# Kernel tuning notes

Measured on AMD Instinct MI355X. Metric: run time of the kernel, lower is better.

The kernel has to match this reference:

```python
import jax, jax.numpy as jnp
import numpy as np

B, L, D, H = 1024, 77, 1024, 16
DFF = 4096


def setup_inputs() -> dict:
    key = jax.random.key(0)
    ks = jax.random.split(key, 26)
    w = lambda k, shape: jax.random.normal(k, shape, jnp.float32) * 0.02
    z = lambda n: jnp.zeros((n,), jnp.float32)
    return {
        "x": jax.random.normal(ks[0], (B, D), jnp.float32),
        "t_emb": jax.random.normal(ks[1], (B, D), jnp.float32),
        "context_seq": jax.random.normal(ks[2], (B, L, D), jnp.float32),
        "context_padding_mask": jnp.zeros((B, L), dtype=bool),
        "w_mod": w(ks[3], (9 * D, D)), "b_mod": z(9 * D),
        "sa_wq": w(ks[4], (D, D)), "sa_bq": z(D),
        "sa_wk": w(ks[5], (D, D)), "sa_bk": z(D),
        "sa_wv": w(ks[6], (D, D)), "sa_bv": z(D),
        "sa_wo": w(ks[7], (D, D)), "sa_bo": z(D),
        "ca_wq": w(ks[8], (D, D)), "ca_bq": z(D),
        "ca_wk": w(ks[9], (D, D)), "ca_bk": z(D),
        "ca_wv": w(ks[10], (D, D)), "ca_bv": z(D),
        "ca_wo": w(ks[11], (D, D)), "ca_bo": z(D),
        "w1": w(ks[12], (DFF, D)), "b1": z(DFF),
        "w2": w(ks[13], (DFF, DFF)), "b2": z(DFF),
        "w3": w(ks[14], (D, DFF)), "b3": z(D),
        "num_heads": H,
    }


def _ln(x, eps=1e-6):
    # LayerNorm without affine params (elementwise_affine=False)
    m = jnp.mean(x, axis=-1, keepdims=True)
    v = jnp.mean(jnp.square(x - m), axis=-1, keepdims=True)
    return (x - m) / jnp.sqrt(v + eps)


def _mha(qx, kx, vx, wq, bq, wk, bk, wv, bv, wo, bo, h, key_padding_mask=None):
    # qx: [B, Lq, D], kx/vx: [B, Lk, D]; torch MultiheadAttention math
    Bb, Lq, Dm = qx.shape
    Lk = kx.shape[1]
    dh = Dm // h
    q = (qx @ wq.T + bq).reshape(Bb, Lq, h, dh).transpose(0, 2, 1, 3)
    k = (kx @ wk.T + bk).reshape(Bb, Lk, h, dh).transpose(0, 2, 1, 3)
    v = (vx @ wv.T + bv).reshape(Bb, Lk, h, dh).transpose(0, 2, 1, 3)
    scores = jnp.einsum("bhqd,bhkd->bhqk", q, k) / jnp.sqrt(jnp.asarray(dh, qx.dtype))
    if key_padding_mask is not None:
        # True means "ignore this key"
        scores = jnp.where(key_padding_mask[:, None, None, :], jnp.asarray(-1e9, qx.dtype), scores)
    attn = jax.nn.softmax(scores, axis=-1)
    out = jnp.einsum("bhqk,bhkd->bhqd", attn, v)
    out = out.transpose(0, 2, 1, 3).reshape(Bb, Lq, Dm)
    return out @ wo.T + bo


def reference(x, t_emb, context_seq, context_padding_mask,
              w_mod, b_mod,
              sa_wq, sa_bq, sa_wk, sa_bk, sa_wv, sa_bv, sa_wo, sa_bo,
              ca_wq, ca_bq, ca_wk, ca_bk, ca_wv, ca_bv, ca_wo, ca_bo,
              w1, b1, w2, b2, w3, b3, num_heads):
    # AdaLN-zero modulation parameters
    mod = jax.nn.silu(t_emb) @ w_mod.T + b_mod  # [B, 9D]
    g1, be1, a1, g2, be2, a2, g3, be3, a3 = jnp.split(mod, 9, axis=1)

    x_q = x[:, None, :]  # [B, 1, D]

    # self-attention branch (seq_len = 1)
    m1 = _ln(x_q) * (1.0 + g1[:, None, :]) + be1[:, None, :]
    sa = _mha(m1, m1, m1, sa_wq, sa_bq, sa_wk, sa_bk, sa_wv, sa_bv, sa_wo, sa_bo, num_heads)
    x_q = x_q + a1[:, None, :] * sa

    # cross-attention branch
    m2 = _ln(x_q) * (1.0 + g2[:, None, :]) + be2[:, None, :]
    ca = _mha(m2, context_seq, context_seq, ca_wq, ca_bq, ca_wk, ca_bk, ca_wv, ca_bv,
              ca_wo, ca_bo, num_heads, key_padding_mask=context_padding_mask)
    x_q = x_q + a2[:, None, :] * ca

    # MLP branch (3-layer, exact GELU as nn.GELU default)
    m3 = _ln(x_q) * (1.0 + g3[:, None, :]) + be3[:, None, :]
    hdn = jax.nn.gelu(m3 @ w1.T + b1, approximate=False)
    hdn = jax.nn.gelu(hdn @ w2.T + b2, approximate=False)
    ff = hdn @ w3.T + b3
    x_q = x_q + a3[:, None, :] * ff

    return x_q[:, 0, :]
```

## Files before the change

### kernel.cpp

```cpp
#include <hip/hip_runtime.h>
#include <cmath>
#include <stdint.h>


#define DD 1024
#define NB 1024
#define LK 77
#define NHEAD 16
#define DFF_ 4096

typedef __bf16 bf16_t;
typedef __attribute__((ext_vector_type(8))) __bf16 bf16x8;
typedef __attribute__((ext_vector_type(4))) __bf16 bf16x4v;
typedef __attribute__((ext_vector_type(4))) float f32x4;

__global__ __launch_bounds__(256) void k_f2b(const float* __restrict__ in,
                                             bf16_t* __restrict__ out, int n) {
    int i = (blockIdx.x * 256 + threadIdx.x) * 4;
    if (i + 3 < n) {
        float4 v = *(const float4*)(in + i);
        bf16x4v o;
        o[0] = (bf16_t)v.x; o[1] = (bf16_t)v.y; o[2] = (bf16_t)v.z; o[3] = (bf16_t)v.w;
        *(bf16x4v*)(out + i) = o;
    }
}

__global__ __launch_bounds__(256) void k_silu_f2b(const float* __restrict__ in,
                                                  bf16_t* __restrict__ out, int n) {
    int i = (blockIdx.x * 256 + threadIdx.x) * 4;
    if (i + 3 < n) {
        float4 v = *(const float4*)(in + i);
        bf16x4v o;
        o[0] = (bf16_t)(v.x / (1.0f + __expf(-v.x)));
        o[1] = (bf16_t)(v.y / (1.0f + __expf(-v.y)));
        o[2] = (bf16_t)(v.z / (1.0f + __expf(-v.z)));
        o[3] = (bf16_t)(v.w / (1.0f + __expf(-v.w)));
        *(bf16x4v*)(out + i) = o;
    }
}

__global__ __launch_bounds__(256) void k_transpose_f2b(const float* __restrict__ in,
                                                       bf16_t* __restrict__ out) {
    __shared__ float t[32][33];
    int lx = threadIdx.x & 31, ly = threadIdx.x >> 5;
    int bx = blockIdx.x * 32, by = blockIdx.y * 32;
#pragma unroll
    for (int r = 0; r < 4; ++r)
        t[ly + r * 8][lx] = in[(size_t)(by + ly + r * 8) * DD + bx + lx];
    __syncthreads();
#pragma unroll
    for (int r = 0; r < 4; ++r)
        out[(size_t)(bx + ly + r * 8) * DD + by + lx] = (bf16_t)t[lx][ly + r * 8];
}

__global__ __launch_bounds__(256) void k_ln_mod(const float* __restrict__ x,
                                                const float* __restrict__ mod,
                                                int gOff, int beOff,
                                                bf16_t* __restrict__ out) {
    const int b = blockIdx.x;
    const int t = threadIdx.x;
    const float4 v = *(const float4*)(x + (size_t)b * DD + t * 4);
    float s = v.x + v.y + v.z + v.w;
    float q = v.x * v.x + v.y * v.y + v.z * v.z + v.w * v.w;
#pragma unroll
    for (int o = 32; o > 0; o >>= 1) {
        s += __shfl_xor(s, o, 64);
        q += __shfl_xor(q, o, 64);
    }
    __shared__ float rs[4], rq[4];
    const int w = t >> 6;
    if ((t & 63) == 0) { rs[w] = s; rq[w] = q; }
    __syncthreads();
    const float S = rs[0] + rs[1] + rs[2] + rs[3];
    const float Q = rq[0] + rq[1] + rq[2] + rq[3];
    const float mean = S * (1.0f / DD);
    const float var = Q * (1.0f / DD) - mean * mean;
    const float rstd = rsqrtf(var + 1e-6f);
    const float* mrow = mod + (size_t)b * (9 * DD);
    const float4 g = *(const float4*)(mrow + gOff + t * 4);
    const float4 e = *(const float4*)(mrow + beOff + t * 4);
    bf16x4v o;
    o[0] = (bf16_t)((v.x - mean) * rstd * (1.0f + g.x) + e.x);
    o[1] = (bf16_t)((v.y - mean) * rstd * (1.0f + g.y) + e.y);
    o[2] = (bf16_t)((v.z - mean) * rstd * (1.0f + g.z) + e.z);
    o[3] = (bf16_t)((v.w - mean) * rstd * (1.0f + g.w) + e.w);
    *(bf16x4v*)(out + (size_t)b * DD + t * 4) = o;
}

template <int BN, bool GELU_E, bool RESID, bool WF32, bool WB16>
__global__ __launch_bounds__(256) void k_gemm(
    const bf16_t* __restrict__ A, int lda, int aHeadOff,
    const bf16_t* __restrict__ W, int ldw, int wHeadOff,
    const float* __restrict__ bias, int biasHeadOff,
    float* __restrict__ Cf, bf16_t* __restrict__ Cb, int ldc, int cHeadOff,
    const float* __restrict__ res, int ldres,
    const float* __restrict__ am, int ldam,
    int K) {
    constexpr int BM = 128, BK = 32;
    const int z = blockIdx.z;
    A += (size_t)z * aHeadOff;
    W += (size_t)z * wHeadOff;
    const float* biasz = bias ? bias + (size_t)z * biasHeadOff : nullptr;
    const size_t coff = (size_t)z * cHeadOff;

    __shared__ bf16_t As[BM * BK];
    __shared__ bf16_t Bs[BN * BK];

    const int tid = threadIdx.x;
    const int wave = tid >> 6, lane = tid & 63;
    const int m0 = blockIdx.y * BM, n0 = blockIdx.x * BN;
    const int wm = (wave >> 1) * 64;
    constexpr int WN = (BN == 128) ? 64 : 32;
    const int wn = (wave & 1) * WN;
    constexpr int FN = WN / 16;

    f32x4 acc[4][FN];
#pragma unroll
    for (int i = 0; i < 4; ++i)
#pragma unroll
        for (int j = 0; j < FN; ++j) acc[i][j] = {0.f, 0.f, 0.f, 0.f};

    const int lrow = lane & 15;
    const int lk8 = (lane >> 4) * 8;

    for (int k0 = 0; k0 < K; k0 += BK) {
        const int c0 = tid, c1 = tid + 256;
        bf16x8 ta0 = *(const bf16x8*)(A + (size_t)(m0 + (c0 >> 2)) * lda + k0 + (c0 & 3) * 8);
        bf16x8 ta1 = *(const bf16x8*)(A + (size_t)(m0 + (c1 >> 2)) * lda + k0 + (c1 & 3) * 8);
        bf16x8 tb0 = *(const bf16x8*)(W + (size_t)(n0 + (c0 >> 2)) * ldw + k0 + (c0 & 3) * 8);
        bf16x8 tb1;
        if constexpr (BN == 128)
            tb1 = *(const bf16x8*)(W + (size_t)(n0 + (c1 >> 2)) * ldw + k0 + (c1 & 3) * 8);

        __syncthreads();
        *(bf16x8*)(As + c0 * 8) = ta0;
        *(bf16x8*)(As + c1 * 8) = ta1;
        *(bf16x8*)(Bs + c0 * 8) = tb0;
        if constexpr (BN == 128) *(bf16x8*)(Bs + c1 * 8) = tb1;
        __syncthreads();

        bf16x8 af[4], bfr[FN];
#pragma unroll
        for (int i = 0; i < 4; ++i)
            af[i] = *(const bf16x8*)(As + (wm + i * 16 + lrow) * BK + lk8);
#pragma unroll
        for (int j = 0; j < FN; ++j)
            bfr[j] = *(const bf16x8*)(Bs + (wn + j * 16 + lrow) * BK + lk8);
#pragma unroll
        for (int i = 0; i < 4; ++i)
#pragma unroll
            for (int j = 0; j < FN; ++j)
                acc[i][j] = __builtin_amdgcn_mfma_f32_16x16x32_bf16(af[i], bfr[j], acc[i][j], 0, 0, 0);
    }

    const int r4 = (lane >> 4) * 4;
    const int cc = lane & 15;
#pragma unroll
    for (int i = 0; i < 4; ++i) {
#pragma unroll
        for (int j = 0; j < FN; ++j) {
            const int col = n0 + wn + j * 16 + cc;
            const float bv = biasz ? biasz[col] : 0.0f;
#pragma unroll
            for (int e = 0; e < 4; ++e) {
                const int row = m0 + wm + i * 16 + r4 + e;
                float v = acc[i][j][e] + bv;
                if constexpr (GELU_E) v = 0.5f * v * (1.0f + erff(v * 0.70710678118654752f));
                const size_t cidx = coff + (size_t)row * ldc + col;
                if constexpr (RESID) {
                    Cf[cidx] = res[(size_t)row * ldres + col] + am[(size_t)row * ldam + col] * v;
                } else {
                    if constexpr (WF32) Cf[cidx] = v;
                    if constexpr (WB16) Cb[cidx] = (bf16_t)v;
                }
            }
        }
    }
}

__global__ __launch_bounds__(64) void k_qbk(const bf16_t* __restrict__ q,
                                            const float* __restrict__ bk,
                                            float* __restrict__ qbk) {
    const int b = blockIdx.x, lane = threadIdx.x;
#pragma unroll 1
    for (int h = 0; h < NHEAD; ++h) {
        float v = (float)q[(size_t)b * DD + h * 64 + lane] * bk[h * 64 + lane];
#pragma unroll
        for (int o = 32; o > 0; o >>= 1) v += __shfl_xor(v, o, 64);
        if (lane == 0) qbk[(size_t)b * NHEAD + h] = v;
    }
}

__global__ __launch_bounds__(256) void k_ca_scores(
    const bf16_t* __restrict__ qt, const float* __restrict__ qbk,
    const float* __restrict__ ctx, const unsigned char* __restrict__ mask,
    float* __restrict__ p) {
    constexpr int QS = DD + 8;
    constexpr int CS = DD + 8;
    __shared__ unsigned short qlds[NHEAD * QS];
    __shared__ float clds[4 * CS];
    __shared__ float slds[NHEAD * 80];
    __shared__ float plds[4 * NHEAD * 4];

    const int b = blockIdx.x;
    const int t = threadIdx.x;
    const unsigned short* qg = (const unsigned short*)(qt + (size_t)b * (NHEAD * DD));
    for (int e = t; e < NHEAD * DD; e += 256) {
        int h = e >> 10, d = e & (DD - 1);
        qlds[h * QS + d] = qg[e];
    }

    const int h = t & 15;
    const int lc = (t >> 4) & 3;
    const int dq = t >> 6;

    for (int c0 = 0; c0 < LK; c0 += 4) {
        __syncthreads();
        {
            int i = t >> 6;
            int dcol = (t & 63) * 16;
            int l = c0 + i;
            if (l < LK) {
                const float* src = ctx + ((size_t)b * LK + l) * DD + dcol;
                float* dst = clds + i * CS + dcol;
#pragma unroll
                for (int u = 0; u < 4; ++u) *(f32x4*)(dst + u * 4) = *(const f32x4*)(src + u * 4);
            }
        }
        __syncthreads();
        int l = c0 + lc;
        float part = 0.0f;
        if (l < LK) {
            const unsigned short* qr = qlds + h * QS + dq * 256;
            const float* cr = clds + lc * CS + dq * 256;
#pragma unroll 4
            for (int d = 0; d < 256; d += 8) {
                bf16x8 qv = *(const bf16x8*)(qr + d);
                f32x4 ca = *(const f32x4*)(cr + d);
                f32x4 cb = *(const f32x4*)(cr + d + 4);
                part += (float)qv[0] * ca.x + (float)qv[1] * ca.y + (float)qv[2] * ca.z +
                        (float)qv[3] * ca.w + (float)qv[4] * cb.x + (float)qv[5] * cb.y +
                        (float)qv[6] * cb.z + (float)qv[7] * cb.w;
            }
        }
        plds[(dq * NHEAD + h) * 4 + lc] = part;
        __syncthreads();
        if (t < 64) {
            int hh = t & 15, ll = t >> 4;
            int lg = c0 + ll;
            if (lg < LK) {
                float s = plds[(0 * NHEAD + hh) * 4 + ll] + plds[(1 * NHEAD + hh) * 4 + ll] +
                          plds[(2 * NHEAD + hh) * 4 + ll] + plds[(3 * NHEAD + hh) * 4 + ll];
                s = (s + qbk[(size_t)b * NHEAD + hh]) * 0.125f;
                if (mask[(size_t)b * LK + lg]) s = -1.0e9f;
                slds[hh * 80 + lg] = s;
            }
        }
    }
    __syncthreads();
    if (t < NHEAD) {
        float mx = -3.0e38f;
#pragma unroll 1
        for (int l2 = 0; l2 < LK; ++l2) mx = fmaxf(mx, slds[t * 80 + l2]);
        float sum = 0.0f;
#pragma unroll 1
        for (int l2 = 0; l2 < LK; ++l2) {
            float e2 = __expf(slds[t * 80 + l2] - mx);
            slds[t * 80 + l2] = e2;
            sum += e2;
        }
        float inv = 1.0f / sum;
#pragma unroll 1
        for (int l2 = 0; l2 < LK; ++l2)
            p[((size_t)b * NHEAD + t) * LK + l2] = slds[t * 80 + l2] * inv;
    }
}

__global__ __launch_bounds__(256) void k_ca_mix(const float* __restrict__ p,
                                                const float* __restrict__ ctx,
                                                bf16_t* __restrict__ mixed) {
    __shared__ float plds[NHEAD * LK];
    __shared__ float clds[4 * DD];
    const int b = blockIdx.x;
    const int t = threadIdx.x;
    for (int e = t; e < NHEAD * LK; e += 256) plds[e] = p[(size_t)b * NHEAD * LK + e];
    const int h = t >> 4, dseg = t & 15;
    f32x4 acc4[16];
#pragma unroll
    for (int j = 0; j < 16; ++j) acc4[j] = {0.f, 0.f, 0.f, 0.f};
    for (int c0 = 0; c0 < LK; c0 += 4) {
        __syncthreads();
        {
            int i = t >> 6;
            int dcol = (t & 63) * 16;
            int l = c0 + i;
            if (l < LK) {
                const float* src = ctx + ((size_t)b * LK + l) * DD + dcol;
                float* dst = clds + i * DD + dcol;
#pragma unroll
                for (int u = 0; u < 4; ++u) *(f32x4*)(dst + u * 4) = *(const f32x4*)(src + u * 4);
            }
        }
        __syncthreads();
#pragma unroll
        for (int lc2 = 0; lc2 < 4; ++lc2) {
            int l = c0 + lc2;
            if (l < LK) {
                float pl = plds[h * LK + l];
                const float* cr = clds + lc2 * DD + dseg * 4;
#pragma unroll
                for (int j = 0; j < 16; ++j) {
                    f32x4 cv = *(const f32x4*)(cr + j * 64);
                    acc4[j].x += pl * cv.x;
                    acc4[j].y += pl * cv.y;
                    acc4[j].z += pl * cv.z;
                    acc4[j].w += pl * cv.w;
                }
            }
        }
    }
    bf16_t* orow = mixed + ((size_t)b * NHEAD + h) * DD + dseg * 4;
#pragma unroll
    for (int j = 0; j < 16; ++j) {
        bf16x4v o;
        o[0] = (bf16_t)acc4[j].x; o[1] = (bf16_t)acc4[j].y;
        o[2] = (bf16_t)acc4[j].z; o[3] = (bf16_t)acc4[j].w;
        *(bf16x4v*)(orow + j * 64) = o;
    }
}

extern "C" void kernel_launch(void* const* d_in, const int* in_sizes, int n_in,
                              void* d_out, int out_size, void* d_ws, size_t ws_size,
                              hipStream_t stream) {
    const float* x = (const float*)d_in[0];
    const float* temb = (const float*)d_in[1];
    const float* ctx = (const float*)d_in[2];
    const unsigned char* mask = (const unsigned char*)d_in[3];
    const float* w_mod = (const float*)d_in[4];
    const float* b_mod = (const float*)d_in[5];
    const float* sa_wv = (const float*)d_in[10];
    const float* sa_bv = (const float*)d_in[11];
    const float* sa_wo = (const float*)d_in[12];
    const float* sa_bo = (const float*)d_in[13];
    const float* ca_wq = (const float*)d_in[14];
    const float* ca_bq = (const float*)d_in[15];
    const float* ca_wk = (const float*)d_in[16];
    const float* ca_bk = (const float*)d_in[17];
    const float* ca_wv = (const float*)d_in[18];
    const float* ca_bv = (const float*)d_in[19];
    const float* ca_wo = (const float*)d_in[20];
    const float* ca_bo = (const float*)d_in[21];
    const float* w1 = (const float*)d_in[22];
    const float* b1 = (const float*)d_in[23];
    const float* w2 = (const float*)d_in[24];
    const float* b2 = (const float*)d_in[25];
    const float* w3 = (const float*)d_in[26];
    const float* b3 = (const float*)d_in[27];

    char* ws = (char*)d_ws;
    size_t off = 0;
    auto alloc = [&](size_t bytes) -> void* {
        void* pp = ws + off;
        off += (bytes + 255) & ~(size_t)255;
        return pp;
    };
    bf16_t* w_mod_b = (bf16_t*)alloc((size_t)9 * DD * DD * 2);
    bf16_t* sa_wv_b = (bf16_t*)alloc((size_t)DD * DD * 2);
    bf16_t* sa_wo_b = (bf16_t*)alloc((size_t)DD * DD * 2);
    bf16_t* ca_wq_b = (bf16_t*)alloc((size_t)DD * DD * 2);
    bf16_t* ca_wv_b = (bf16_t*)alloc((size_t)DD * DD * 2);
    bf16_t* ca_wo_b = (bf16_t*)alloc((size_t)DD * DD * 2);
    bf16_t* wkT_b = (bf16_t*)alloc((size_t)DD * DD * 2);
    bf16_t* w1_b = (bf16_t*)alloc((size_t)DFF_ * DD * 2);
    bf16_t* w2_b = (bf16_t*)alloc((size_t)DFF_ * DFF_ * 2);
    bf16_t* w3_b = (bf16_t*)alloc((size_t)DD * DFF_ * 2);
    bf16_t* tb = (bf16_t*)alloc((size_t)NB * DD * 2);
    float* mod_f = (float*)alloc((size_t)NB * 9 * DD * 4);
    bf16_t* m_b = (bf16_t*)alloc((size_t)NB * DD * 2);
    bf16_t* vsa_b = (bf16_t*)alloc((size_t)NB * DD * 2);
    float* x1 = (float*)alloc((size_t)NB * DD * 4);
    float* x2 = (float*)alloc((size_t)NB * DD * 4);
    bf16_t* q_b = (bf16_t*)alloc((size_t)NB * DD * 2);
    bf16_t* qt_b = (bf16_t*)alloc((size_t)NB * NHEAD * DD * 2);
    float* qbk_f = (float*)alloc((size_t)NB * NHEAD * 4);
    float* p_f = (float*)alloc((size_t)NB * NHEAD * LK * 4);
    bf16_t* oh_b = (bf16_t*)alloc((size_t)NB * DD * 2);
    bf16_t* h1_b = (bf16_t*)alloc((size_t)NB * DFF_ * 2);
    bf16_t* h2_b = (bf16_t*)alloc((size_t)NB * DFF_ * 2);
    bf16_t* mixed_b = qt_b;
    (void)n_in; (void)in_sizes; (void)out_size; (void)ws_size;

    dim3 blk(256);
    k_f2b<<<9 * DD * DD / 1024, blk, 0, stream>>>(w_mod, w_mod_b, 9 * DD * DD);
    k_f2b<<<DD * DD / 1024, blk, 0, stream>>>(sa_wv, sa_wv_b, DD * DD);
    k_f2b<<<DD * DD / 1024, blk, 0, stream>>>(sa_wo, sa_wo_b, DD * DD);
    k_f2b<<<DD * DD / 1024, blk, 0, stream>>>(ca_wq, ca_wq_b, DD * DD);
    k_f2b<<<DD * DD / 1024, blk, 0, stream>>>(ca_wv, ca_wv_b, DD * DD);
    k_f2b<<<DD * DD / 1024, blk, 0, stream>>>(ca_wo, ca_wo_b, DD * DD);
    k_f2b<<<DFF_ * DD / 1024, blk, 0, stream>>>(w1, w1_b, DFF_ * DD);
    k_f2b<<<DFF_ * DFF_ / 1024, blk, 0, stream>>>(w2, w2_b, DFF_ * DFF_);
    k_f2b<<<DFF_ * DD / 1024, blk, 0, stream>>>(w3, w3_b, DFF_ * DD);
    k_transpose_f2b<<<dim3(32, 32), blk, 0, stream>>>(ca_wk, wkT_b);
    k_silu_f2b<<<NB * DD / 1024, blk, 0, stream>>>(temb, tb, NB * DD);

    k_gemm<128, false, false, true, false><<<dim3(9 * DD / 128, NB / 128, 1), blk, 0, stream>>>(
        tb, DD, 0, w_mod_b, DD, 0, b_mod, 0, mod_f, nullptr, 9 * DD, 0, nullptr, 0, nullptr, 0, DD);

    k_ln_mod<<<NB, blk, 0, stream>>>(x, mod_f, 0 * DD, 1 * DD, m_b);
    k_gemm<128, false, false, false, true><<<dim3(8, 8, 1), blk, 0, stream>>>(
        m_b, DD, 0, sa_wv_b, DD, 0, sa_bv, 0, nullptr, vsa_b, DD, 0, nullptr, 0, nullptr, 0, DD);
    k_gemm<128, false, true, true, false><<<dim3(8, 8, 1), blk, 0, stream>>>(
        vsa_b, DD, 0, sa_wo_b, DD, 0, sa_bo, 0, x1, nullptr, DD, 0, x, DD, mod_f + 2 * DD, 9 * DD, DD);

    k_ln_mod<<<NB, blk, 0, stream>>>(x1, mod_f, 3 * DD, 4 * DD, m_b);
    k_gemm<128, false, false, false, true><<<dim3(8, 8, 1), blk, 0, stream>>>(
        m_b, DD, 0, ca_wq_b, DD, 0, ca_bq, 0, nullptr, q_b, DD, 0, nullptr, 0, nullptr, 0, DD);
    k_gemm<128, false, false, false, true><<<dim3(8, 8, 16), blk, 0, stream>>>(
        q_b, DD, 64, wkT_b, DD, 64, nullptr, 0, nullptr, qt_b, NHEAD * DD, DD, nullptr, 0, nullptr, 0, 64);
    k_qbk<<<NB, 64, 0, stream>>>(q_b, ca_bk, qbk_f);
    k_ca_scores<<<NB, blk, 0, stream>>>(qt_b, qbk_f, ctx, mask, p_f);
    k_ca_mix<<<NB, blk, 0, stream>>>(p_f, ctx, mixed_b);
    k_gemm<64, false, false, false, true><<<dim3(1, 8, 16), blk, 0, stream>>>(
        mixed_b, NHEAD * DD, DD, ca_wv_b, DD, 64 * DD, ca_bv, 64, nullptr, oh_b, DD, 64,
        nullptr, 0, nullptr, 0, DD);
    k_gemm<128, false, true, true, false><<<dim3(8, 8, 1), blk, 0, stream>>>(
        oh_b, DD, 0, ca_wo_b, DD, 0, ca_bo, 0, x2, nullptr, DD, 0, x1, DD, mod_f + 5 * DD, 9 * DD, DD);

    k_ln_mod<<<NB, blk, 0, stream>>>(x2, mod_f, 6 * DD, 7 * DD, m_b);
    k_gemm<128, true, false, false, true><<<dim3(DFF_ / 128, 8, 1), blk, 0, stream>>>(
        m_b, DD, 0, w1_b, DD, 0, b1, 0, nullptr, h1_b, DFF_, 0, nullptr, 0, nullptr, 0, DD);
    k_gemm<128, true, false, false, true><<<dim3(DFF_ / 128, 8, 1), blk, 0, stream>>>(
        h1_b, DFF_, 0, w2_b, DFF_, 0, b2, 0, nullptr, h2_b, DFF_, 0, nullptr, 0, nullptr, 0, DFF_);
    k_gemm<128, false, true, true, false><<<dim3(8, 8, 1), blk, 0, stream>>>(
        h2_b, DFF_, 0, w3_b, DFF_, 0, b3, 0, (float*)d_out, nullptr, DD, 0, x2, DD,
        mod_f + 8 * DD, 9 * DD, DFF_);
}
```

Measured before the change: 1.251 ms.

## Fuse cross-attention into online-softmax kernel, batch weight casts, retile GEMMs with direct LDS loads

```diff
diff --git a/kernel.cpp b/kernel.cpp
--- a/kernel.cpp
+++ b/kernel.cpp
@@ -14,29 +14,31 @@
 typedef __attribute__((ext_vector_type(4))) __bf16 bf16x4v;
 typedef __attribute__((ext_vector_type(4))) float f32x4;
 
-__global__ __launch_bounds__(256) void k_f2b(const float* __restrict__ in,
-                                             bf16_t* __restrict__ out, int n) {
-    int i = (blockIdx.x * 256 + threadIdx.x) * 4;
-    if (i + 3 < n) {
-        float4 v = *(const float4*)(in + i);
-        bf16x4v o;
-        o[0] = (bf16_t)v.x; o[1] = (bf16_t)v.y; o[2] = (bf16_t)v.z; o[3] = (bf16_t)v.w;
-        *(bf16x4v*)(out + i) = o;
-    }
-}
-
-__global__ __launch_bounds__(256) void k_silu_f2b(const float* __restrict__ in,
-                                                  bf16_t* __restrict__ out, int n) {
-    int i = (blockIdx.x * 256 + threadIdx.x) * 4;
-    if (i + 3 < n) {
-        float4 v = *(const float4*)(in + i);
-        bf16x4v o;
-        o[0] = (bf16_t)(v.x / (1.0f + __expf(-v.x)));
-        o[1] = (bf16_t)(v.y / (1.0f + __expf(-v.y)));
-        o[2] = (bf16_t)(v.z / (1.0f + __expf(-v.z)));
-        o[3] = (bf16_t)(v.w / (1.0f + __expf(-v.w)));
-        *(bf16x4v*)(out + i) = o;
-    }
+__device__ __forceinline__ void gload16(const bf16_t* g, bf16_t* l) {
+    __builtin_amdgcn_global_load_lds(
+        (const __attribute__((address_space(1))) void*)g,
+        (__attribute__((address_space(3))) void*)l, 16, 0, 0);
+}
+
+struct ConvTab {
+    const float* src[40];
+    bf16_t* dst[40];
+    int silu[40];
+};
+
+__global__ __launch_bounds__(256) void k_conv_all(ConvTab tab) {
+    const int u = blockIdx.x >> 10;
+    const int i = ((blockIdx.x & 1023) * 256 + threadIdx.x) * 4;
+    float4 v = *(const float4*)(tab.src[u] + i);
+    if (tab.silu[u]) {
+        v.x = v.x / (1.0f + __expf(-v.x));
+        v.y = v.y / (1.0f + __expf(-v.y));
+        v.z = v.z / (1.0f + __expf(-v.z));
+        v.w = v.w / (1.0f + __expf(-v.w));
+    }
+    bf16x4v o;
+    o[0] = (bf16_t)v.x; o[1] = (bf16_t)v.y; o[2] = (bf16_t)v.z; o[3] = (bf16_t)v.w;
+    *(bf16x4v*)(tab.dst[u] + i) = o;
 }
 
 __global__ __launch_bounds__(256) void k_transpose_f2b(const float* __restrict__ in,
@@ -87,7 +89,7 @@
     *(bf16x4v*)(out + (size_t)b * DD + t * 4) = o;
 }
 
-template <int BN, bool GELU_E, bool RESID, bool WF32, bool WB16>
+template <int BM, int BN, bool GELU_E, bool RESID, bool WF32, bool WB16>
 __global__ __launch_bounds__(256) void k_gemm(
     const bf16_t* __restrict__ A, int lda, int aHeadOff,
     const bf16_t* __restrict__ W, int ldw, int wHeadOff,
@@ -96,7 +98,10 @@
     const float* __restrict__ res, int ldres,
     const float* __restrict__ am, int ldam,
     int K) {
-    constexpr int BM = 128, BK = 32;
+    constexpr int BK = 32;
+    constexpr int FM = BM / 32, FN = BN / 32;
+    constexpr int CA_ = (BM * BK) / 2048;
+    constexpr int CB_ = (BN * BK) / 2048;
     const int z = blockIdx.z;
     A += (size_t)z * aHeadOff;
     W += (size_t)z * wHeadOff;
@@ -109,14 +114,12 @@
     const int tid = threadIdx.x;
     const int wave = tid >> 6, lane = tid & 63;
     const int m0 = blockIdx.y * BM, n0 = blockIdx.x * BN;
-    const int wm = (wave >> 1) * 64;
-    constexpr int WN = (BN == 128) ? 64 : 32;
-    const int wn = (wave & 1) * WN;
-    constexpr int FN = WN / 16;
-
-    f32x4 acc[4][FN];
-#pragma unroll
-    for (int i = 0; i < 4; ++i)
+    const int wm = (wave >> 1) * (BM / 2);
+    const int wn = (wave & 1) * (BN / 2);
+
+    f32x4 acc[FM][FN];
+#pragma unroll
+    for (int i = 0; i < FM; ++i)
 #pragma unroll
         for (int j = 0; j < FN; ++j) acc[i][j] = {0.f, 0.f, 0.f, 0.f};
 
@@ -124,30 +127,28 @@
     const int lk8 = (lane >> 4) * 8;
 
     for (int k0 = 0; k0 < K; k0 += BK) {
-        const int c0 = tid, c1 = tid + 256;
-        bf16x8 ta0 = *(const bf16x8*)(A + (size_t)(m0 + (c0 >> 2)) * lda + k0 + (c0 & 3) * 8);
-        bf16x8 ta1 = *(const bf16x8*)(A + (size_t)(m0 + (c1 >> 2)) * lda + k0 + (c1 & 3) * 8);
-        bf16x8 tb0 = *(const bf16x8*)(W + (size_t)(n0 + (c0 >> 2)) * ldw + k0 + (c0 & 3) * 8);
-        bf16x8 tb1;
-        if constexpr (BN == 128)
-            tb1 = *(const bf16x8*)(W + (size_t)(n0 + (c1 >> 2)) * ldw + k0 + (c1 & 3) * 8);
-
-        __syncthreads();
-        *(bf16x8*)(As + c0 * 8) = ta0;
-        *(bf16x8*)(As + c1 * 8) = ta1;
-        *(bf16x8*)(Bs + c0 * 8) = tb0;
-        if constexpr (BN == 128) *(bf16x8*)(Bs + c1 * 8) = tb1;
-        __syncthreads();
-
-        bf16x8 af[4], bfr[FN];
-#pragma unroll
-        for (int i = 0; i < 4; ++i)
+        __syncthreads();
+#pragma unroll
+        for (int c = 0; c < CA_; ++c) {
+            const int e = (c * 256 + tid) * 8;
+            gload16(A + (size_t)(m0 + (e >> 5)) * lda + k0 + (e & 31), As + e);
+        }
+#pragma unroll
+        for (int c = 0; c < CB_; ++c) {
+            const int e = (c * 256 + tid) * 8;
+            gload16(W + (size_t)(n0 + (e >> 5)) * ldw + k0 + (e & 31), Bs + e);
+        }
+        __syncthreads();
+
+        bf16x8 af[FM], bfr[FN];
+#pragma unroll
+        for (int i = 0; i < FM; ++i)
             af[i] = *(const bf16x8*)(As + (wm + i * 16 + lrow) * BK + lk8);
 #pragma unroll
         for (int j = 0; j < FN; ++j)
             bfr[j] = *(const bf16x8*)(Bs + (wn + j * 16 + lrow) * BK + lk8);
 #pragma unroll
-        for (int i = 0; i < 4; ++i)
+        for (int i = 0; i < FM; ++i)
 #pragma unroll
             for (int j = 0; j < FN; ++j)
                 acc[i][j] = __builtin_amdgcn_mfma_f32_16x16x32_bf16(af[i], bfr[j], acc[i][j], 0, 0, 0);
@@ -156,7 +157,7 @@
     const int r4 = (lane >> 4) * 4;
     const int cc = lane & 15;
 #pragma unroll
-    for (int i = 0; i < 4; ++i) {
+    for (int i = 0; i < FM; ++i) {
 #pragma unroll
         for (int j = 0; j < FN; ++j) {
             const int col = n0 + wn + j * 16 + cc;
@@ -191,141 +192,133 @@
     }
 }
 
-__global__ __launch_bounds__(256) void k_ca_scores(
+#define CQS 1032
+__global__ __launch_bounds__(256) void k_ca_fused(
     const bf16_t* __restrict__ qt, const float* __restrict__ qbk,
     const float* __restrict__ ctx, const unsigned char* __restrict__ mask,
-    float* __restrict__ p) {
-    constexpr int QS = DD + 8;
-    constexpr int CS = DD + 8;
-    __shared__ unsigned short qlds[NHEAD * QS];
-    __shared__ float clds[4 * CS];
-    __shared__ float slds[NHEAD * 80];
-    __shared__ float plds[4 * NHEAD * 4];
+    bf16_t* __restrict__ mixed) {
+    __shared__ bf16_t qs[16 * CQS];
+    __shared__ bf16_t cs[8 * CQS];
+    __shared__ float plds[2 * 16 * 8];
+    __shared__ float wex[16 * 8];
+    __shared__ float fs[16];
+    __shared__ float inv[16];
 
     const int b = blockIdx.x;
     const int t = threadIdx.x;
-    const unsigned short* qg = (const unsigned short*)(qt + (size_t)b * (NHEAD * DD));
-    for (int e = t; e < NHEAD * DD; e += 256) {
-        int h = e >> 10, d = e & (DD - 1);
-        qlds[h * QS + d] = qg[e];
-    }
-
-    const int h = t & 15;
-    const int lc = (t >> 4) & 3;
-    const int dq = t >> 6;
-
-    for (int c0 = 0; c0 < LK; c0 += 4) {
+
+    {
+        const int h = t >> 4, dl = (t & 15) * 8;
+        const bf16_t* src = qt + ((size_t)b * 16 + h) * DD;
+#pragma unroll
+        for (int u = 0; u < 8; ++u)
+            *(bf16x8*)(qs + h * CQS + dl + u * 128) = *(const bf16x8*)(src + dl + u * 128);
+    }
+
+    const int hD = t & 15, l3D = (t >> 4) & 7, dq = t >> 7;
+    const int hM = t >> 4, ds16 = t & 15;
+    float acc[8][8];
+#pragma unroll
+    for (int j = 0; j < 8; ++j)
+#pragma unroll
+        for (int e = 0; e < 8; ++e) acc[j][e] = 0.f;
+
+    float mrun = -3.0e38f, den = 0.f;
+    const float qb = (t < 16) ? qbk[(size_t)b * NHEAD + t] : 0.f;
+
+    for (int c0 = 0; c0 < LK; c0 += 8) {
         __syncthreads();
         {
-            int i = t >> 6;
-            int dcol = (t & 63) * 16;
-            int l = c0 + i;
-            if (l < LK) {
-                const float* src = ctx + ((size_t)b * LK + l) * DD + dcol;
-                float* dst = clds + i * CS + dcol;
-#pragma unroll
-                for (int u = 0; u < 4; ++u) *(f32x4*)(dst + u * 4) = *(const f32x4*)(src + u * 4);
-            }
-        }
-        __syncthreads();
-        int l = c0 + lc;
-        float part = 0.0f;
-        if (l < LK) {
-            const unsigned short* qr = qlds + h * QS + dq * 256;
-            const float* cr = clds + lc * CS + dq * 256;
-#pragma unroll 4
-            for (int d = 0; d < 256; d += 8) {
-                bf16x8 qv = *(const bf16x8*)(qr + d);
-                f32x4 ca = *(const f32x4*)(cr + d);
-                f32x4 cb = *(const f32x4*)(cr + d + 4);
-                part += (float)qv[0] * ca.x + (float)qv[1] * ca.y + (float)qv[2] * ca.z +
-                        (float)qv[3] * ca.w + (float)qv[4] * cb.x + (float)qv[5] * cb.y +
-                        (float)qv[6] * cb.z + (float)qv[7] * cb.w;
-            }
-        }
-        plds[(dq * NHEAD + h) * 4 + lc] = part;
-        __syncthreads();
-        if (t < 64) {
-            int hh = t & 15, ll = t >> 4;
-            int lg = c0 + ll;
+            const int l = t >> 5, d4 = (t & 31) * 4;
+            const int lg = c0 + l;
             if (lg < LK) {
-                float s = plds[(0 * NHEAD + hh) * 4 + ll] + plds[(1 * NHEAD + hh) * 4 + ll] +
-                          plds[(2 * NHEAD + hh) * 4 + ll] + plds[(3 * NHEAD + hh) * 4 + ll];
-                s = (s + qbk[(size_t)b * NHEAD + hh]) * 0.125f;
-                if (mask[(size_t)b * LK + lg]) s = -1.0e9f;
-                slds[hh * 80 + lg] = s;
+                const float* src = ctx + ((size_t)b * LK + lg) * DD;
+#pragma unroll
+                for (int u = 0; u < 8; ++u) {
+                    f32x4 v = *(const f32x4*)(src + d4 + u * 128);
+                    bf16x4v o;
+                    o[0] = (bf16_t)v.x; o[1] = (bf16_t)v.y;
+                    o[2] = (bf16_t)v.z; o[3] = (bf16_t)v.w;
+                    *(bf16x4v*)(cs + l * CQS + d4 + u * 128) = o;
+                }
+            } else {
+                bf16x4v o = {(bf16_t)0.f, (bf16_t)0.f, (bf16_t)0.f, (bf16_t)0.f};
+#pragma unroll
+                for (int u = 0; u < 8; ++u) *(bf16x4v*)(cs + l * CQS + d4 + u * 128) = o;
+            }
+        }
+        __syncthreads();
+        {
+            float part = 0.f;
+            const bf16_t* qr = qs + hD * CQS + dq * 512;
+            const bf16_t* cr = cs + l3D * CQS + dq * 512;
+#pragma unroll 8
+            for (int i = 0; i < 64; ++i) {
+                bf16x8 qv = *(const bf16x8*)(qr + i * 8);
+                bf16x8 cv = *(const bf16x8*)(cr + i * 8);
+#pragma unroll
+                for (int e = 0; e < 8; ++e) part += (float)qv[e] * (float)cv[e];
+            }
+            plds[dq * 128 + hD * 8 + l3D] = part;
+        }
+        __syncthreads();
+        if (t < 16) {
+            float s[8];
+            float cm = -3.0e38f;
+#pragma unroll
+            for (int l = 0; l < 8; ++l) {
+                const int lg = c0 + l;
+                float sv = -3.0e38f;
+                if (lg < LK) {
+                    sv = (plds[t * 8 + l] + plds[128 + t * 8 + l] + qb) * 0.125f;
+                    if (mask[(size_t)b * LK + lg]) sv = -1.0e9f;
+                }
+                s[l] = sv;
+                cm = fmaxf(cm, sv);
+            }
+            const float mnew = fmaxf(mrun, cm);
+            const float f = __expf(mrun - mnew);
+            float wsum = 0.f;
+#pragma unroll
+            for (int l = 0; l < 8; ++l) {
+                const float w = (c0 + l < LK) ? __expf(s[l] - mnew) : 0.f;
+                wex[t * 8 + l] = w;
+                wsum += w;
+            }
+            den = den * f + wsum;
+            mrun = mnew;
+            fs[t] = f;
+            inv[t] = 1.0f / den;
+        }
+        __syncthreads();
+        {
+            const float f = fs[hM];
+#pragma unroll
+            for (int j = 0; j < 8; ++j)
+#pragma unroll
+                for (int e = 0; e < 8; ++e) acc[j][e] *= f;
+#pragma unroll
+            for (int l = 0; l < 8; ++l) {
+                const float w = wex[hM * 8 + l];
+                const bf16_t* cr = cs + l * CQS + ds16 * 8;
+#pragma unroll
+                for (int j = 0; j < 8; ++j) {
+                    bf16x8 cv = *(const bf16x8*)(cr + j * 128);
+#pragma unroll
+                    for (int e = 0; e < 8; ++e) acc[j][e] += w * (float)cv[e];
+                }
             }
         }
     }
     __syncthreads();
-    if (t < NHEAD) {
-        float mx = -3.0e38f;
-#pragma unroll 1
-        for (int l2 = 0; l2 < LK; ++l2) mx = fmaxf(mx, slds[t * 80 + l2]);
-        float sum = 0.0f;
-#pragma unroll 1
-        for (int l2 = 0; l2 < LK; ++l2) {
-            float e2 = __expf(slds[t * 80 + l2] - mx);
-            slds[t * 80 + l2] = e2;
-            sum += e2;
-        }
-        float inv = 1.0f / sum;
-#pragma unroll 1
-        for (int l2 = 0; l2 < LK; ++l2)
-            p[((size_t)b * NHEAD + t) * LK + l2] = slds[t * 80 + l2] * inv;
-    }
-}
-
-__global__ __launch_bounds__(256) void k_ca_mix(const float* __restrict__ p,
-                                                const float* __restrict__ ctx,
-                                                bf16_t* __restrict__ mixed) {
-    __shared__ float plds[NHEAD * LK];
-    __shared__ float clds[4 * DD];
-    const int b = blockIdx.x;
-    const int t = threadIdx.x;
-    for (int e = t; e < NHEAD * LK; e += 256) plds[e] = p[(size_t)b * NHEAD * LK + e];
-    const int h = t >> 4, dseg = t & 15;
-    f32x4 acc4[16];
-#pragma unroll
-    for (int j = 0; j < 16; ++j) acc4[j] = {0.f, 0.f, 0.f, 0.f};
-    for (int c0 = 0; c0 < LK; c0 += 4) {
-        __syncthreads();
-        {
-            int i = t >> 6;
-            int dcol = (t & 63) * 16;
-            int l = c0 + i;
-            if (l < LK) {
-                const float* src = ctx + ((size_t)b * LK + l) * DD + dcol;
-                float* dst = clds + i * DD + dcol;
-#pragma unroll
-                for (int u = 0; u < 4; ++u) *(f32x4*)(dst + u * 4) = *(const f32x4*)(src + u * 4);
-            }
-        }
-        __syncthreads();
-#pragma unroll
-        for (int lc2 = 0; lc2 < 4; ++lc2) {
-            int l = c0 + lc2;
-            if (l < LK) {
-                float pl = plds[h * LK + l];
-                const float* cr = clds + lc2 * DD + dseg * 4;
-#pragma unroll
-                for (int j = 0; j < 16; ++j) {
-                    f32x4 cv = *(const f32x4*)(cr + j * 64);
-                    acc4[j].x += pl * cv.x;
-                    acc4[j].y += pl * cv.y;
-                    acc4[j].z += pl * cv.z;
-                    acc4[j].w += pl * cv.w;
-                }
-            }
-        }
-    }
-    bf16_t* orow = mixed + ((size_t)b * NHEAD + h) * DD + dseg * 4;
-#pragma unroll
-    for (int j = 0; j < 16; ++j) {
-        bf16x4v o;
-        o[0] = (bf16_t)acc4[j].x; o[1] = (bf16_t)acc4[j].y;
-        o[2] = (bf16_t)acc4[j].z; o[3] = (bf16_t)acc4[j].w;
-        *(bf16x4v*)(orow + j * 64) = o;
+    const float iv = inv[hM];
+    bf16_t* orow = mixed + ((size_t)b * NHEAD + hM) * DD + ds16 * 8;
+#pragma unroll
+    for (int j = 0; j < 8; ++j) {
+        bf16x8 o;
+#pragma unroll
+        for (int e = 0; e < 8; ++e) o[e] = (bf16_t)(acc[j][e] * iv);
+        *(bf16x8*)(orow + j * 128) = o;
     }
 }
 
@@ -383,7 +376,6 @@
     bf16_t* q_b = (bf16_t*)alloc((size_t)NB * DD * 2);
     bf16_t* qt_b = (bf16_t*)alloc((size_t)NB * NHEAD * DD * 2);
     float* qbk_f = (float*)alloc((size_t)NB * NHEAD * 4);
-    float* p_f = (float*)alloc((size_t)NB * NHEAD * LK * 4);
     bf16_t* oh_b = (bf16_t*)alloc((size_t)NB * DD * 2);
     bf16_t* h1_b = (bf16_t*)alloc((size_t)NB * DFF_ * 2);
     bf16_t* h2_b = (bf16_t*)alloc((size_t)NB * DFF_ * 2);
@@ -391,47 +383,57 @@
     (void)n_in; (void)in_sizes; (void)out_size; (void)ws_size;
 
     dim3 blk(256);
-    k_f2b<<<9 * DD * DD / 1024, blk, 0, stream>>>(w_mod, w_mod_b, 9 * DD * DD);
-    k_f2b<<<DD * DD / 1024, blk, 0, stream>>>(sa_wv, sa_wv_b, DD * DD);
-    k_f2b<<<DD * DD / 1024, blk, 0, stream>>>(sa_wo, sa_wo_b, DD * DD);
-    k_f2b<<<DD * DD / 1024, blk, 0, stream>>>(ca_wq, ca_wq_b, DD * DD);
-    k_f2b<<<DD * DD / 1024, blk, 0, stream>>>(ca_wv, ca_wv_b, DD * DD);
-    k_f2b<<<DD * DD / 1024, blk, 0, stream>>>(ca_wo, ca_wo_b, DD * DD);
-    k_f2b<<<DFF_ * DD / 1024, blk, 0, stream>>>(w1, w1_b, DFF_ * DD);
-    k_f2b<<<DFF_ * DFF_ / 1024, blk, 0, stream>>>(w2, w2_b, DFF_ * DFF_);
-    k_f2b<<<DFF_ * DD / 1024, blk, 0, stream>>>(w3, w3_b, DFF_ * DD);
+    ConvTab tab{};
+    int nu = 0;
+    auto addseg = [&](const float* s, bf16_t* d, int units, int silu) {
+        for (int k = 0; k < units; ++k) {
+            tab.src[nu] = s + (size_t)k * 1048576;
+            tab.dst[nu] = d + (size_t)k * 1048576;
+            tab.silu[nu] = silu;
+            ++nu;
+        }
+    };
+    addseg(w_mod, w_mod_b, 9, 0);
+    addseg(sa_wv, sa_wv_b, 1, 0);
+    addseg(sa_wo, sa_wo_b, 1, 0);
+    addseg(ca_wq, ca_wq_b, 1, 0);
+    addseg(ca_wv, ca_wv_b, 1, 0);
+    addseg(ca_wo, ca_wo_b, 1, 0);
+    addseg(w1, w1_b, 4, 0);
+    addseg(w2, w2_b, 16, 0);
+    addseg(w3, w3_b, 4, 0);
+    addseg(temb, tb, 1, 1);
+    k_conv_all<<<nu * 1024, blk, 0, stream>>>(tab);
     k_transpose_f2b<<<dim3(32, 32), blk, 0, stream>>>(ca_wk, wkT_b);
-    k_silu_f2b<<<NB * DD / 1024, blk, 0, stream>>>(temb, tb, NB * DD);
-
-    k_gemm<128, false, false, true, false><<<dim3(9 * DD / 128, NB / 128, 1), blk, 0, stream>>>(
+
+    k_gemm<128, 128, false, false, true, false><<<dim3(72, 8, 1), blk, 0, stream>>>(
         tb, DD, 0, w_mod_b, DD, 0, b_mod, 0, mod_f, nullptr, 9 * DD, 0, nullptr, 0, nullptr, 0, DD);
 
     k_ln_mod<<<NB, blk, 0, stream>>>(x, mod_f, 0 * DD, 1 * DD, m_b);
-    k_gemm<128, false, false, false, true><<<dim3(8, 8, 1), blk, 0, stream>>>(
+    k_gemm<64, 64, false, false, false, true><<<dim3(16, 16, 1), blk, 0, stream>>>(
         m_b, DD, 0, sa_wv_b, DD, 0, sa_bv, 0, nullptr, vsa_b, DD, 0, nullptr, 0, nullptr, 0, DD);
-    k_gemm<128, false, true, true, false><<<dim3(8, 8, 1), blk, 0, stream>>>(
+    k_gemm<64, 64, false, true, true, false><<<dim3(16, 16, 1), blk, 0, stream>>>(
         vsa_b, DD, 0, sa_wo_b, DD, 0, sa_bo, 0, x1, nullptr, DD, 0, x, DD, mod_f + 2 * DD, 9 * DD, DD);
 
     k_ln_mod<<<NB, blk, 0, stream>>>(x1, mod_f, 3 * DD, 4 * DD, m_b);
-    k_gemm<128, false, false, false, true><<<dim3(8, 8, 1), blk, 0, stream>>>(
+    k_gemm<64, 64, false, false, false, true><<<dim3(16, 16, 1), blk, 0, stream>>>(
         m_b, DD, 0, ca_wq_b, DD, 0, ca_bq, 0, nullptr, q_b, DD, 0, nullptr, 0, nullptr, 0, DD);
-    k_gemm<128, false, false, false, true><<<dim3(8, 8, 16), blk, 0, stream>>>(
+    k_gemm<64, 64, false, false, false, true><<<dim3(16, 16, 16), blk, 0, stream>>>(
         q_b, DD, 64, wkT_b, DD, 64, nullptr, 0, nullptr, qt_b, NHEAD * DD, DD, nullptr, 0, nullptr, 0, 64);
     k_qbk<<<NB, 64, 0, stream>>>(q_b, ca_bk, qbk_f);
-    k_ca_scores<<<NB, blk, 0, stream>>>(qt_b, qbk_f, ctx, mask, p_f);
-    k_ca_mix<<<NB, blk, 0, stream>>>(p_f, ctx, mixed_b);
-    k_gemm<64, false, false, false, true><<<dim3(1, 8, 16), blk, 0, stream>>>(
+    k_ca_fused<<<NB, blk, 0, stream>>>(qt_b, qbk_f, ctx, mask, mixed_b);
+    k_gemm<64, 64, false, false, false, true><<<dim3(1, 16, 16), blk, 0, stream>>>(
         mixed_b, NHEAD * DD, DD, ca_wv_b, DD, 64 * DD, ca_bv, 64, nullptr, oh_b, DD, 64,
         nullptr, 0, nullptr, 0, DD);
-    k_gemm<128, false, true, true, false><<<dim3(8, 8, 1), blk, 0, stream>>>(
+    k_gemm<64, 64, false, true, true, false><<<dim3(16, 16, 1), blk, 0, stream>>>(
         oh_b, DD, 0, ca_wo_b, DD, 0, ca_bo, 0, x2, nullptr, DD, 0, x1, DD, mod_f + 5 * DD, 9 * DD, DD);
 
     k_ln_mod<<<NB, blk, 0, stream>>>(x2, mod_f, 6 * DD, 7 * DD, m_b);
-    k_gemm<128, true, false, false, true><<<dim3(DFF_ / 128, 8, 1), blk, 0, stream>>>(
+    k_gemm<64, 128, true, false, false, true><<<dim3(32, 16, 1), blk, 0, stream>>>(
         m_b, DD, 0, w1_b, DD, 0, b1, 0, nullptr, h1_b, DFF_, 0, nullptr, 0, nullptr, 0, DD);
-    k_gemm<128, true, false, false, true><<<dim3(DFF_ / 128, 8, 1), blk, 0, stream>>>(
+    k_gemm<64, 128, true, false, false, true><<<dim3(32, 16, 1), blk, 0, stream>>>(
         h1_b, DFF_, 0, w2_b, DFF_, 0, b2, 0, nullptr, h2_b, DFF_, 0, nullptr, 0, nullptr, 0, DFF_);
-    k_gemm<128, false, true, true, false><<<dim3(8, 8, 1), blk, 0, stream>>>(
+    k_gemm<64, 64, false, true, true, false><<<dim3(16, 16, 1), blk, 0, stream>>>(
         h2_b, DFF_, 0, w3_b, DFF_, 0, b3, 0, (float*)d_out, nullptr, DD, 0, x2, DD,
         mod_f + 8 * DD, 9 * DD, DFF_);
 }
```

Result: faster. 1.192 ms (-4.7%).
